# Optimization experiments

Measured on AMD Instinct MI355X. Metric: run time of the kernel, lower is better.

## Reference

```python
import jax, jax.numpy as jnp
import numpy as np

EPS = 1e-7      # geometric epsilon used in LOAI_features
BN_EPS = 1e-5   # torch BatchNorm default eps (eval mode)
B, N, C = 8, 8192, 2
S, K = 1024, 32
C_PREV = 64


def _index_points(points, idx):
    # points [B,N,C], idx [B,S,K] int -> [B,S,K,C] (torch index_points)
    return jax.vmap(lambda p, i: p[i])(points, idx)


def _conv_bn_relu(x, w, b, g, beta, m, v):
    # 1x1 Conv2d + eval-mode BatchNorm2d + ReLU. x [B,Cin,K,S], w [Cout,Cin]
    y = jnp.einsum('bcks,oc->boks', x, w) + b[None, :, None, None]
    scale = g * jax.lax.rsqrt(v + BN_EPS)
    y = (y - m[None, :, None, None]) * scale[None, :, None, None] + beta[None, :, None, None]
    return jax.nn.relu(y)


def setup_inputs() -> dict:
    key = jax.random.key(0)
    ks = jax.random.split(key, 8)
    contour = jax.random.normal(ks[0], (B, N, C), jnp.float32)
    loa = jax.random.normal(ks[1], (B, N, C), jnp.float32)
    loa = loa / (jnp.linalg.norm(loa, axis=-1, keepdims=True) + 1e-8)  # unit LOA vectors
    prev = jax.random.normal(ks[2], (B, C_PREV, N), jnp.float32)

    def lin(k, o, i):
        return jax.random.normal(k, (o, i), jnp.float32) * (1.0 / np.sqrt(i))

    d = {
        'contour_all_points': contour,
        'LOA_all_points': loa,
        'feature_maps_from_prev_layer': prev,
        # feature-enhancement MLP: 8 -> 32 -> 64
        'ew1': lin(ks[3], 32, 8), 'eb1': jnp.zeros(32), 'eg1': jnp.ones(32),
        'ebeta1': jnp.zeros(32), 'em1': jnp.zeros(32), 'ev1': jnp.ones(32),
        'ew2': lin(ks[4], 64, 32), 'eb2': jnp.zeros(64), 'eg2': jnp.ones(64),
        'ebeta2': jnp.zeros(64), 'em2': jnp.zeros(64), 'ev2': jnp.ones(64),
        # filter MLP: (64 + C_PREV)=128 -> 128 -> 256
        'fw1': lin(ks[5], 128, 64 + C_PREV), 'fb1': jnp.zeros(128), 'fg1': jnp.ones(128),
        'fbeta1': jnp.zeros(128), 'fm1': jnp.zeros(128), 'fv1': jnp.ones(128),
        'fw2': lin(ks[6], 256, 128), 'fb2': jnp.zeros(256), 'fg2': jnp.ones(256),
        'fbeta2': jnp.zeros(256), 'fm2': jnp.zeros(256), 'fv2': jnp.ones(256),
    }
    return d


def reference(contour_all_points, LOA_all_points, feature_maps_from_prev_layer,
              ew1, eb1, eg1, ebeta1, em1, ev1,
              ew2, eb2, eg2, ebeta2, em2, ev2,
              fw1, fb1, fg1, fbeta1, fm1, fv1,
              fw2, fb2, fg2, fbeta2, fm2, fv2):
    # --- downsampling: linspace indices over contour (static) ---
    new_idx = np.linspace(0, N - 1, S).astype(np.int64)              # [S]
    gidx_np = (new_idx[None, :, None] - K // 2 + np.arange(K)[None, None, :]) % N  # [1,S,K]
    gidx = jnp.broadcast_to(jnp.asarray(gidx_np), (B, S, K))

    sampled = contour_all_points[:, new_idx, :]                      # [B,S,C]
    loa_ci = LOA_all_points[:, new_idx, :][:, :, None, :]            # [B,S,1,C]

    # --- gather neighbor windows ---
    xi = _index_points(contour_all_points, gidx)                     # [B,S,K,C]
    loa_xi = _index_points(LOA_all_points, gidx)                     # [B,S,K,C]

    def sdot(a, b):
        return jnp.sum(a * b, axis=-1, keepdims=True)

    def oriented_angle(cos_a, cos_b, dotp):
        ang = jnp.arccos(jnp.clip(dotp, -1.0 + EPS, 1.0 - EPS))
        sign = jnp.where(cos_a < cos_b, 1.0, -1.0)  # equal case -> -1, as in torch
        return sign * ang

    # --- rotation-invariant features ---
    vec = xi - sampled[:, :, None, :]
    f4 = jnp.linalg.norm(vec, axis=-1, keepdims=True)                # dist ci->xi
    u = vec / (f4 + EPS)
    a1 = sdot(loa_ci, u)
    a2 = sdot(loa_xi, -u)
    f3o = oriented_angle(a1, a2, sdot(loa_xi, loa_ci))

    vecp = xi - jnp.roll(xi, 1, axis=2)
    vecp = vecp.at[:, :, 0, :].set(0.0)
    f8 = jnp.linalg.norm(vecp, axis=-1, keepdims=True)
    up = vecp / (f8 + EPS)
    loa_xim1 = jnp.roll(loa_xi, 1, axis=2).at[:, :, 0, :].set(0.0)
    a4 = sdot(up, loa_xi)
    a5 = sdot(up, loa_xim1)
    f7o = oriented_angle(a4, a5, sdot(loa_xi, loa_xim1))

    ru = jnp.roll(u, 1, axis=2).at[:, :, 0, :].set(0.0)
    d2 = jnp.arccos(jnp.clip(sdot(u, ru), -1.0 + EPS, 1.0 - EPS))

    rif = jnp.concatenate([f4, d2, a1, a2, f3o, a4, a5, f7o], axis=-1)  # [B,S,K,8]

    # --- feature enhancement MLP on [B,8,K,S] ---
    x = jnp.transpose(rif, (0, 3, 2, 1))
    x = _conv_bn_relu(x, ew1, eb1, eg1, ebeta1, em1, ev1)
    x = _conv_bn_relu(x, ew2, eb2, eg2, ebeta2, em2, ev2)            # [B,64,K,S]

    # --- group previous-layer features and concat ---
    prev_bnc = jnp.transpose(feature_maps_from_prev_layer, (0, 2, 1))  # [B,N,Cp]
    grouped_prev = _index_points(prev_bnc, gidx)                     # [B,S,K,Cp]
    grouped_prev = jnp.transpose(grouped_prev, (0, 3, 2, 1))         # [B,Cp,K,S]
    x = jnp.concatenate([x, grouped_prev], axis=1)                   # [B,128,K,S]

    # --- filter MLP + max-pool over neighbors ---
    x = _conv_bn_relu(x, fw1, fb1, fg1, fbeta1, fm1, fv1)
    x = _conv_bn_relu(x, fw2, fb2, fg2, fbeta2, fm2, fv2)            # [B,256,K,S]
    out = jnp.max(x, axis=2)                                         # [B,256,S]
    return out
```

## Files before the change

kernel.cpp:

```cpp
#include <hip/hip_runtime.h>
#include <math.h>

namespace {

constexpr int Nn = 8192;
constexpr int Ss = 1024;
constexpr float F_EPS = 1e-7f;
constexpr float F_BN_EPS = 1e-5f;

typedef __attribute__((ext_vector_type(8))) short s16x8;
typedef __attribute__((ext_vector_type(4))) float f32x4;

constexpr int WB3 = 0;
constexpr int WB4 = 32768;
constexpr int BB3 = 98304;
constexpr int BB4 = 98816;
constexpr int EW1 = 99840;
constexpr int EB1 = 100864;
constexpr int EW2 = 100992;
constexpr int EB2 = 109184;
constexpr size_t WS_NEED = 109440;

constexpr size_t CATO = 131072;
constexpr size_t PVT  = CATO + 33554432ull;
constexpr size_t WS_BIG = PVT + 8388608ull;

__device__ inline unsigned short f2bf(float f) {
  unsigned int u = __builtin_bit_cast(unsigned int, f);
  u += 0x7fffu + ((u >> 16) & 1u);
  return (unsigned short)(u >> 16);
}

__device__ inline s16x8 pack_scaled(const float* __restrict__ p, float sc) {
  const float4 w0 = *(const float4*)p;
  const float4 w1 = *(const float4*)(p + 4);
  s16x8 r;
  r[0] = (short)f2bf(w0.x * sc); r[1] = (short)f2bf(w0.y * sc);
  r[2] = (short)f2bf(w0.z * sc); r[3] = (short)f2bf(w0.w * sc);
  r[4] = (short)f2bf(w1.x * sc); r[5] = (short)f2bf(w1.y * sc);
  r[6] = (short)f2bf(w1.z * sc); r[7] = (short)f2bf(w1.w * sc);
  return r;
}

__device__ inline s16x8 prev_frag(const float* __restrict__ prev, int b, int cbase, int n) {
  const float* p = prev + (size_t)(b * 64 + cbase) * Nn + n;
  s16x8 r;
#pragma unroll
  for (int j = 0; j < 8; ++j) r[j] = (short)f2bf(p[j * Nn]);
  return r;
}

__device__ inline int ci_of(int s) {
  return (s == Ss - 1) ? (Nn - 1) : (int)(long long)((double)s * (8191.0 / 1023.0));
}

__global__ __launch_bounds__(256) void rcri_prep(
    const float* __restrict__ ew1, const float* __restrict__ eb1,
    const float* __restrict__ eg1, const float* __restrict__ ebeta1,
    const float* __restrict__ em1, const float* __restrict__ ev1,
    const float* __restrict__ ew2, const float* __restrict__ eb2,
    const float* __restrict__ eg2, const float* __restrict__ ebeta2,
    const float* __restrict__ em2, const float* __restrict__ ev2,
    const float* __restrict__ fw1, const float* __restrict__ fb1,
    const float* __restrict__ fg1, const float* __restrict__ fbeta1,
    const float* __restrict__ fm1, const float* __restrict__ fv1,
    const float* __restrict__ fw2, const float* __restrict__ fb2,
    const float* __restrict__ fg2, const float* __restrict__ fbeta2,
    const float* __restrict__ fm2, const float* __restrict__ fv2,
    unsigned char* __restrict__ ws)
{
  const int i = blockIdx.x * 256 + threadIdx.x;
  if (i < 16384) {
    const int o = i >> 7;
    const float sc = fg1[o] * rsqrtf(fv1[o] + F_BN_EPS);
    ((unsigned short*)(ws + WB3))[i] = f2bf(fw1[i] * sc);
    return;
  }
  int j = i - 16384;
  if (j < 32768) {
    const int o = j >> 7;
    const float sc = fg2[o] * rsqrtf(fv2[o] + F_BN_EPS);
    ((unsigned short*)(ws + WB4))[j] = f2bf(fw2[j] * sc);
    return;
  }
  j -= 32768;
  if (j < 128) {
    const float sc = fg1[j] * rsqrtf(fv1[j] + F_BN_EPS);
    ((float*)(ws + BB3))[j] = (fb1[j] - fm1[j]) * sc + fbeta1[j];
    return;
  }
  j -= 128;
  if (j < 256) {
    const float sc = fg2[j] * rsqrtf(fv2[j] + F_BN_EPS);
    ((float*)(ws + BB4))[j] = (fb2[j] - fm2[j]) * sc + fbeta2[j];
    return;
  }
  j -= 256;
  if (j < 256) {
    const int o = j >> 3;
    const float sc = eg1[o] * rsqrtf(ev1[o] + F_BN_EPS);
    ((float*)(ws + EW1))[j] = ew1[j] * sc;
    return;
  }
  j -= 256;
  if (j < 32) {
    const float sc = eg1[j] * rsqrtf(ev1[j] + F_BN_EPS);
    ((float*)(ws + EB1))[j] = (eb1[j] - em1[j]) * sc + ebeta1[j];
    return;
  }
  j -= 32;
  if (j < 2048) {
    const int o = j >> 5;
    const float sc = eg2[o] * rsqrtf(ev2[o] + F_BN_EPS);
    ((float*)(ws + EW2))[j] = ew2[j] * sc;
    return;
  }
  j -= 2048;
  if (j < 64) {
    const float sc = eg2[j] * rsqrtf(ev2[j] + F_BN_EPS);
    ((float*)(ws + EB2))[j] = (eb2[j] - em2[j]) * sc + ebeta2[j];
  }
}

__global__ __launch_bounds__(256) void rcri_tpose(
    const float* __restrict__ prev, unsigned char* __restrict__ ws)
{
  __shared__ unsigned short tile[128 * 72];
  const int t = threadIdx.x;
  const int b = blockIdx.x >> 6;
  const int n0 = (blockIdx.x & 63) * 128;
  const int nloc = t & 127;
  const int chalf = t >> 7;

#pragma unroll
  for (int it = 0; it < 32; ++it) {
    const int c = it * 2 + chalf;
    const float v = prev[(size_t)(b * 64 + c) * Nn + n0 + nloc];
    tile[nloc * 72 + c] = f2bf(v);
  }
  __syncthreads();

#pragma unroll
  for (int it = 0; it < 4; ++it) {
    const int idx = it * 256 + t;
    const int rn = idx >> 3;
    const int cc = idx & 7;
    const uint4 v = *(const uint4*)((const unsigned char*)tile + rn * 144 + cc * 16);
    *(uint4*)(ws + PVT + (size_t)(b * Nn + n0 + rn) * 128 + cc * 16) = v;
  }
}

__global__ __launch_bounds__(256) void rcri_k1f2(
    const float* __restrict__ contour, const float* __restrict__ loa,
    unsigned char* __restrict__ ws)
{
  __shared__ float wlds[2400];
  __shared__ __align__(16) unsigned char cstage[128 * 144];

  const int t = threadIdx.x;
  for (int j = t; j < 2400; j += 256) wlds[j] = ((const float*)(ws + EW1))[j];

  const int r = t & 127;
  const int hf = t >> 7;
  const int row = blockIdx.x * 128 + r;
  const int b = row >> 15;
  const int s = (row >> 5) & 1023;
  const int kk = row & 31;
  const int ci = ci_of(s);
  const int n = (ci - 16 + kk) & (Nn - 1);

  const float2* c2 = (const float2*)contour;
  const float2* l2 = (const float2*)loa;

  const float2 xi = c2[b * Nn + n];
  const float2 lx = l2[b * Nn + n];
  const float2 sp = c2[b * Nn + ci];
  const float2 lc = l2[b * Nn + ci];

  float2 xim1 = make_float2(0.f, 0.f), lxm1 = make_float2(0.f, 0.f);
  if (kk > 0) {
    const int np = (ci - 16 + kk - 1) & (Nn - 1);
    xim1 = c2[b * Nn + np];
    lxm1 = l2[b * Nn + np];
  }

  const float vx = xi.x - sp.x, vy = xi.y - sp.y;
  const float f4 = sqrtf(vx * vx + vy * vy);
  const float inv = 1.0f / (f4 + F_EPS);
  const float ux = vx * inv, uy = vy * inv;
  const float a1 = lc.x * ux + lc.y * uy;
  const float a2 = -(lx.x * ux + lx.y * uy);
  float dotp = lx.x * lc.x + lx.y * lc.y;
  float cl = fminf(fmaxf(dotp, -1.0f + F_EPS), 1.0f - F_EPS);
  const float f3o = (a1 < a2 ? 1.0f : -1.0f) * acosf(cl);

  float pux = 0.f, puy = 0.f;
  if (kk > 0) {
    const float pvx = xim1.x - sp.x, pvy = xim1.y - sp.y;
    const float pf4 = sqrtf(pvx * pvx + pvy * pvy);
    const float pinv = 1.0f / (pf4 + F_EPS);
    pux = pvx * pinv; puy = pvy * pinv;
  }
  const float vpx = (kk > 0) ? (xi.x - xim1.x) : 0.0f;
  const float vpy = (kk > 0) ? (xi.y - xim1.y) : 0.0f;
  const float f8 = sqrtf(vpx * vpx + vpy * vpy);
  const float invp = 1.0f / (f8 + F_EPS);
  const float upx = vpx * invp, upy = vpy * invp;
  const float a4 = upx * lx.x + upy * lx.y;
  const float a5 = upx * lxm1.x + upy * lxm1.y;
  float dotp2 = lx.x * lxm1.x + lx.y * lxm1.y;
  float cl2 = fminf(fmaxf(dotp2, -1.0f + F_EPS), 1.0f - F_EPS);
  const float f7o = (a4 < a5 ? 1.0f : -1.0f) * acosf(cl2);
  float du = ux * pux + uy * puy;
  float cl3 = fminf(fmaxf(du, -1.0f + F_EPS), 1.0f - F_EPS);
  const float d2 = acosf(cl3);

  __syncthreads();

  float h1v[32];
#pragma unroll
  for (int o = 0; o < 32; ++o) {
    const float4 w0 = *(const float4*)(wlds + o * 8);
    const float4 w1 = *(const float4*)(wlds + o * 8 + 4);
    float acc = wlds[256 + o]
      + w0.x * f4  + w0.y * d2  + w0.z * a1  + w0.w * a2
      + w1.x * f3o + w1.y * a4  + w1.z * a5  + w1.w * f7o;
    h1v[o] = fmaxf(acc, 0.f);
  }

#pragma unroll
  for (int grp = 0; grp < 4; ++grp) {
    unsigned int uu[4];
#pragma unroll
    for (int q = 0; q < 4; ++q) {
      float y2[2];
#pragma unroll
      for (int jj = 0; jj < 2; ++jj) {
        const int o = hf * 32 + grp * 8 + q * 2 + jj;
        float acc = wlds[2336 + o];
#pragma unroll
        for (int c4 = 0; c4 < 8; ++c4) {
          const float4 ww = *(const float4*)(wlds + 288 + o * 32 + c4 * 4);
          acc += ww.x * h1v[c4 * 4 + 0] + ww.y * h1v[c4 * 4 + 1]
               + ww.z * h1v[c4 * 4 + 2] + ww.w * h1v[c4 * 4 + 3];
        }
        y2[jj] = fmaxf(acc, 0.f);
      }
      uu[q] = (unsigned)f2bf(y2[0]) | ((unsigned)f2bf(y2[1]) << 16);
    }
    *(uint4*)(cstage + r * 144 + hf * 64 + grp * 16) = make_uint4(uu[0], uu[1], uu[2], uu[3]);
  }
  __syncthreads();

#pragma unroll
  for (int it = 0; it < 4; ++it) {
    const int idx = it * 256 + t;
    const int rr = idx >> 3;
    const int cc = idx & 7;
    const uint4 v = *(const uint4*)(cstage + rr * 144 + cc * 16);
    *(uint4*)(ws + CATO + (size_t)(blockIdx.x * 128 + rr) * 128 + cc * 16) = v;
  }
}

__global__ __launch_bounds__(256) void rcri_k23(
    const unsigned char* __restrict__ ws, float* __restrict__ out)
{
  __shared__ __align__(16) unsigned char h3s[32768];
  __shared__ float obuf[256 * 5];

  const int t = threadIdx.x;
  const int lane = t & 63;
  const int w = t >> 6;
  const int rl = lane & 15;
  const int g = lane >> 4;
  const int rows0 = blockIdx.x * 128;
  const int b = blockIdx.x >> 8;
  const int sbase = (blockIdx.x & 255) * 4;

  {
    const unsigned short* wb3 = (const unsigned short*)(ws + WB3);
    const float* b3p = (const float*)(ws + BB3);
    s16x8 B3[2][4];
    float bb3[2];
#pragma unroll
    for (int i = 0; i < 2; ++i) {
      const int o = (2 * w + i) * 16 + rl;
#pragma unroll
      for (int kt = 0; kt < 4; ++kt)
        B3[i][kt] = *(const s16x8*)(wb3 + o * 128 + kt * 32 + 8 * g);
      bb3[i] = b3p[o];
    }
    for (int mt = 0; mt < 8; ++mt) {
      const int row = rows0 + mt * 16 + rl;
      const int s = (row >> 5) & 1023;
      const int kk = row & 31;
      const int ci = ci_of(s);
      const int n = (ci - 16 + kk) & (Nn - 1);

      const s16x8 a0 = __builtin_bit_cast(s16x8,
          *(const uint4*)(ws + CATO + (size_t)row * 128 + 16 * g));
      const s16x8 a1 = __builtin_bit_cast(s16x8,
          *(const uint4*)(ws + CATO + (size_t)row * 128 + 64 + 16 * g));
      const s16x8 a2 = __builtin_bit_cast(s16x8,
          *(const uint4*)(ws + PVT + (size_t)(b * Nn + n) * 128 + 16 * g));
      const s16x8 a3 = __builtin_bit_cast(s16x8,
          *(const uint4*)(ws + PVT + (size_t)(b * Nn + n) * 128 + 64 + 16 * g));

#pragma unroll
      for (int i = 0; i < 2; ++i) {
        f32x4 acc = {0.f, 0.f, 0.f, 0.f};
        acc = __builtin_amdgcn_mfma_f32_16x16x32_bf16(a0, B3[i][0], acc, 0, 0, 0);
        acc = __builtin_amdgcn_mfma_f32_16x16x32_bf16(a1, B3[i][1], acc, 0, 0, 0);
        acc = __builtin_amdgcn_mfma_f32_16x16x32_bf16(a2, B3[i][2], acc, 0, 0, 0);
        acc = __builtin_amdgcn_mfma_f32_16x16x32_bf16(a3, B3[i][3], acc, 0, 0, 0);
        const int o = (2 * w + i) * 16 + rl;
#pragma unroll
        for (int r = 0; r < 4; ++r) {
          const int row2 = mt * 16 + 4 * g + r;
          const float y = fmaxf(acc[r] + bb3[i], 0.f);
          *(unsigned short*)(h3s + row2 * 256 + ((2 * o) ^ ((row2 & 15) << 4))) = f2bf(y);
        }
      }
    }
  }
  __syncthreads();

  {
    const unsigned short* wb4 = (const unsigned short*)(ws + WB4);
    const float* b4p = (const float*)(ws + BB4);
    s16x8 B4[4][4];
    float bb4[4];
#pragma unroll
    for (int ni = 0; ni < 4; ++ni) {
      const int o = (4 * w + ni) * 16 + rl;
#pragma unroll
      for (int kt = 0; kt < 4; ++kt)
        B4[ni][kt] = *(const s16x8*)(wb4 + o * 128 + kt * 32 + 8 * g);
      bb4[ni] = b4p[o];
    }
    float vmax[4] = {-INFINITY, -INFINITY, -INFINITY, -INFINITY};
    for (int mt = 0; mt < 8; ++mt) {
      const int rowl = mt * 16 + rl;
      s16x8 a[4];
#pragma unroll
      for (int kt = 0; kt < 4; ++kt)
        a[kt] = __builtin_bit_cast(s16x8,
            *(const uint4*)(h3s + rowl * 256 + ((kt * 64 + 16 * g) ^ ((rowl & 15) << 4))));
#pragma unroll
      for (int ni = 0; ni < 4; ++ni) {
        f32x4 acc = {0.f, 0.f, 0.f, 0.f};
        acc = __builtin_amdgcn_mfma_f32_16x16x32_bf16(a[0], B4[ni][0], acc, 0, 0, 0);
        acc = __builtin_amdgcn_mfma_f32_16x16x32_bf16(a[1], B4[ni][1], acc, 0, 0, 0);
        acc = __builtin_amdgcn_mfma_f32_16x16x32_bf16(a[2], B4[ni][2], acc, 0, 0, 0);
        acc = __builtin_amdgcn_mfma_f32_16x16x32_bf16(a[3], B4[ni][3], acc, 0, 0, 0);
#pragma unroll
        for (int r = 0; r < 4; ++r)
          vmax[ni] = fmaxf(vmax[ni], fmaxf(acc[r] + bb4[ni], 0.f));
      }
      if (mt & 1) {
        const int sl = mt >> 1;
#pragma unroll
        for (int ni = 0; ni < 4; ++ni) {
          float v = vmax[ni];
          v = fmaxf(v, __shfl_xor(v, 16));
          v = fmaxf(v, __shfl_xor(v, 32));
          if (g == 0) {
            const int o = (4 * w + ni) * 16 + rl;
            obuf[o * 5 + sl] = v;
          }
          vmax[ni] = -INFINITY;
        }
      }
    }
  }
  __syncthreads();
  {
    float v[4];
#pragma unroll
    for (int j = 0; j < 4; ++j) v[j] = obuf[t * 5 + j];
    float* po = out + ((size_t)(b * 256 + t) << 10) + sbase;
    float4 v0; v0.x = v[0]; v0.y = v[1]; v0.z = v[2]; v0.w = v[3];
    *(float4*)po = v0;
  }
}

template <bool P>
__global__ __launch_bounds__(256, 2) void rcri_main(
    const float* __restrict__ contour, const float* __restrict__ loa,
    const float* __restrict__ prev, const unsigned char* __restrict__ ws,
    const float* __restrict__ ew1, const float* __restrict__ eb1,
    const float* __restrict__ eg1, const float* __restrict__ ebeta1,
    const float* __restrict__ em1, const float* __restrict__ ev1,
    const float* __restrict__ ew2, const float* __restrict__ eb2,
    const float* __restrict__ eg2, const float* __restrict__ ebeta2,
    const float* __restrict__ em2, const float* __restrict__ ev2,
    const float* __restrict__ fw1, const float* __restrict__ fb1,
    const float* __restrict__ fg1, const float* __restrict__ fbeta1,
    const float* __restrict__ fm1, const float* __restrict__ fv1,
    const float* __restrict__ fw2, const float* __restrict__ fb2,
    const float* __restrict__ fg2, const float* __restrict__ fbeta2,
    const float* __restrict__ fm2, const float* __restrict__ fv2,
    float* __restrict__ out)
{
  __shared__ __align__(16) unsigned char smem[65536 + 9216];
  float* obuf = (float*)(smem + 65536);

  const int t = threadIdx.x;
  const int lane = t & 63;
  const int w = t >> 6;
  const int rl = lane & 15;
  const int g = lane >> 4;
  const int blk = blockIdx.x;
  const int b = blk >> 7;
  const int s_base = (blk & 127) << 3;

  const unsigned short* wb3 = (const unsigned short*)(ws + WB3);
  const unsigned short* wb4 = (const unsigned short*)(ws + WB4);
  const float* b3p = (const float*)(ws + BB3);
  const float* b4p = (const float*)(ws + BB4);
  const float* w1p = (const float*)(ws + EW1);
  const float* b1p = (const float*)(ws + EB1);
  const float* w2p = (const float*)(ws + EW2);
  const float* b2p = (const float*)(ws + EB2);

  const float2* c2 = (const float2*)contour;
  const float2* l2 = (const float2*)loa;

  auto cat_off = [](int m, int byte) { return m * 256 + (byte ^ ((m & 15) << 4)); };
  auto h3_off  = [](int m, int byte) { return 32768 + m * 256 + (byte ^ ((m & 15) << 4)); };

  for (int hh = 0; hh < 2; ++hh) {
    {
      const int m = t & 127;
      const int hf = t >> 7;
      const int sl4 = m >> 5, kk = m & 31;
      const int s = s_base + hh * 4 + sl4;
      const int ci = ci_of(s);
      const int n = (ci - 16 + kk) & (Nn - 1);

#pragma unroll
      for (int u = 0; u < 8; ++u) {
        const int c0 = hf * 32 + u * 4;
        const float* pp = prev + (size_t)(b * 64 + c0) * Nn + n;
        const float p0 = pp[0], p1 = pp[Nn], p2 = pp[2 * Nn], p3 = pp[3 * Nn];
        const unsigned int u0 = (unsigned)f2bf(p0) | ((unsigned)f2bf(p1) << 16);
        const unsigned int u1 = (unsigned)f2bf(p2) | ((unsigned)f2bf(p3) << 16);
        *(uint2*)(smem + cat_off(m, 128 + 2 * c0)) = make_uint2(u0, u1);
      }

      const float2 xi = c2[b * Nn + n];
      const float2 lx = l2[b * Nn + n];
      const float2 sp = c2[b * Nn + ci];
      const float2 lc = l2[b * Nn + ci];

      float2 xim1 = make_float2(0.f, 0.f), lxm1 = make_float2(0.f, 0.f);
      if (kk > 0) {
        const int np = (ci - 16 + kk - 1) & (Nn - 1);
        xim1 = c2[b * Nn + np];
        lxm1 = l2[b * Nn + np];
      }

      const float vx = xi.x - sp.x, vy = xi.y - sp.y;
      const float f4 = sqrtf(vx * vx + vy * vy);
      const float inv = 1.0f / (f4 + F_EPS);
      const float ux = vx * inv, uy = vy * inv;
      const float a1 = lc.x * ux + lc.y * uy;
      const float a2 = -(lx.x * ux + lx.y * uy);
      float dotp = lx.x * lc.x + lx.y * lc.y;
      float cl = fminf(fmaxf(dotp, -1.0f + F_EPS), 1.0f - F_EPS);
      const float f3o = (a1 < a2 ? 1.0f : -1.0f) * acosf(cl);

      float pux = 0.f, puy = 0.f;
      if (kk > 0) {
        const float pvx = xim1.x - sp.x, pvy = xim1.y - sp.y;
        const float pf4 = sqrtf(pvx * pvx + pvy * pvy);
        const float pinv = 1.0f / (pf4 + F_EPS);
        pux = pvx * pinv; puy = pvy * pinv;
      }
      const float vpx = (kk > 0) ? (xi.x - xim1.x) : 0.0f;
      const float vpy = (kk > 0) ? (xi.y - xim1.y) : 0.0f;
      const float f8 = sqrtf(vpx * vpx + vpy * vpy);
      const float invp = 1.0f / (f8 + F_EPS);
      const float upx = vpx * invp, upy = vpy * invp;
      const float a4 = upx * lx.x + upy * lx.y;
      const float a5 = upx * lxm1.x + upy * lxm1.y;
      float dotp2 = lx.x * lxm1.x + lx.y * lxm1.y;
      float cl2 = fminf(fmaxf(dotp2, -1.0f + F_EPS), 1.0f - F_EPS);
      const float f7o = (a4 < a5 ? 1.0f : -1.0f) * acosf(cl2);
      float du = ux * pux + uy * puy;
      float cl3 = fminf(fmaxf(du, -1.0f + F_EPS), 1.0f - F_EPS);
      const float d2 = acosf(cl3);

      const float rif[8] = {f4, d2, a1, a2, f3o, a4, a5, f7o};

      float h1v[32];
#pragma unroll
      for (int o = 0; o < 32; ++o) {
        float acc;
        if (P) {
          acc = b1p[o];
#pragma unroll
          for (int c = 0; c < 8; ++c) acc += w1p[o * 8 + c] * rif[c];
        } else {
          float a0 = 0.f;
#pragma unroll
          for (int c = 0; c < 8; ++c) a0 += ew1[o * 8 + c] * rif[c];
          const float sc = eg1[o] * rsqrtf(ev1[o] + F_BN_EPS);
          acc = (a0 + eb1[o] - em1[o]) * sc + ebeta1[o];
        }
        h1v[o] = fmaxf(acc, 0.f);
      }

#pragma unroll
      for (int i = 0; i < 8; ++i) {
        float yv[4];
#pragma unroll
        for (int j = 0; j < 4; ++j) {
          const int o = hf * 32 + i * 4 + j;
          float acc;
          if (P) {
            acc = b2p[o];
#pragma unroll
            for (int c = 0; c < 32; ++c) acc += w2p[o * 32 + c] * h1v[c];
          } else {
            float a0 = 0.f;
#pragma unroll
            for (int c = 0; c < 32; ++c) a0 += ew2[o * 32 + c] * h1v[c];
            const float sc = eg2[o] * rsqrtf(ev2[o] + F_BN_EPS);
            acc = (a0 + eb2[o] - em2[o]) * sc + ebeta2[o];
          }
          yv[j] = fmaxf(acc, 0.f);
        }
        const unsigned int u0 = (unsigned)f2bf(yv[0]) | ((unsigned)f2bf(yv[1]) << 16);
        const unsigned int u1 = (unsigned)f2bf(yv[2]) | ((unsigned)f2bf(yv[3]) << 16);
        *(uint2*)(smem + cat_off(m, 64 * hf + 8 * i)) = make_uint2(u0, u1);
      }
    }
    __syncthreads();

    {
      s16x8 B3[2][4];
      float bb3[2];
#pragma unroll
      for (int i = 0; i < 2; ++i) {
        const int o = (2 * w + i) * 16 + rl;
        if (P) {
#pragma unroll
          for (int kt = 0; kt < 4; ++kt)
            B3[i][kt] = *(const s16x8*)(wb3 + o * 128 + kt * 32 + 8 * g);
          bb3[i] = b3p[o];
        } else {
          const float sc = fg1[o] * rsqrtf(fv1[o] + F_BN_EPS);
#pragma unroll
          for (int kt = 0; kt < 4; ++kt)
            B3[i][kt] = pack_scaled(fw1 + o * 128 + kt * 32 + 8 * g, sc);
          bb3[i] = (fb1[o] - fm1[o]) * sc + fbeta1[o];
        }
      }
      for (int mt = 0; mt < 8; ++mt) {
        const int row = mt * 16 + rl;
        s16x8 a[4];
#pragma unroll
        for (int kt = 0; kt < 4; ++kt)
          a[kt] = __builtin_bit_cast(s16x8, *(const uint4*)(smem + cat_off(row, kt * 64 + 16 * g)));
#pragma unroll
        for (int i = 0; i < 2; ++i) {
          f32x4 acc = {0.f, 0.f, 0.f, 0.f};
          acc = __builtin_amdgcn_mfma_f32_16x16x32_bf16(a[0], B3[i][0], acc, 0, 0, 0);
          acc = __builtin_amdgcn_mfma_f32_16x16x32_bf16(a[1], B3[i][1], acc, 0, 0, 0);
          acc = __builtin_amdgcn_mfma_f32_16x16x32_bf16(a[2], B3[i][2], acc, 0, 0, 0);
          acc = __builtin_amdgcn_mfma_f32_16x16x32_bf16(a[3], B3[i][3], acc, 0, 0, 0);
          const int o = (2 * w + i) * 16 + rl;
#pragma unroll
          for (int r = 0; r < 4; ++r) {
            const float y = fmaxf(acc[r] + bb3[i], 0.f);
            *(unsigned short*)(smem + h3_off(mt * 16 + 4 * g + r, 2 * o)) = f2bf(y);
          }
        }
      }
    }
    __syncthreads();

#pragma unroll
    for (int nip = 0; nip < 2; ++nip) {
      s16x8 B4[2][4];
      float bb4[2];
#pragma unroll
      for (int q = 0; q < 2; ++q) {
        const int o = (4 * w + nip * 2 + q) * 16 + rl;
        if (P) {
#pragma unroll
          for (int kt = 0; kt < 4; ++kt)
            B4[q][kt] = *(const s16x8*)(wb4 + o * 128 + kt * 32 + 8 * g);
          bb4[q] = b4p[o];
        } else {
          const float sc = fg2[o] * rsqrtf(fv2[o] + F_BN_EPS);
#pragma unroll
          for (int kt = 0; kt < 4; ++kt)
            B4[q][kt] = pack_scaled(fw2 + o * 128 + kt * 32 + 8 * g, sc);
          bb4[q] = (fb2[o] - fm2[o]) * sc + fbeta2[o];
        }
      }
      float vm[2] = {-INFINITY, -INFINITY};
      for (int mt = 0; mt < 8; ++mt) {
        const int row = mt * 16 + rl;
        s16x8 a[4];
#pragma unroll
        for (int kt = 0; kt < 4; ++kt)
          a[kt] = __builtin_bit_cast(s16x8, *(const uint4*)(smem + h3_off(row, kt * 64 + 16 * g)));
#pragma unroll
        for (int q = 0; q < 2; ++q) {
          f32x4 acc = {0.f, 0.f, 0.f, 0.f};
          acc = __builtin_amdgcn_mfma_f32_16x16x32_bf16(a[0], B4[q][0], acc, 0, 0, 0);
          acc = __builtin_amdgcn_mfma_f32_16x16x32_bf16(a[1], B4[q][1], acc, 0, 0, 0);
          acc = __builtin_amdgcn_mfma_f32_16x16x32_bf16(a[2], B4[q][2], acc, 0, 0, 0);
          acc = __builtin_amdgcn_mfma_f32_16x16x32_bf16(a[3], B4[q][3], acc, 0, 0, 0);
#pragma unroll
          for (int r = 0; r < 4; ++r)
            vm[q] = fmaxf(vm[q], fmaxf(acc[r] + bb4[q], 0.f));
        }
        if (mt & 1) {
          const int sl = hh * 4 + (mt >> 1);
#pragma unroll
          for (int q = 0; q < 2; ++q) {
            float v = vm[q];
            v = fmaxf(v, __shfl_xor(v, 16));
            v = fmaxf(v, __shfl_xor(v, 32));
            if (g == 0) {
              const int o = (4 * w + nip * 2 + q) * 16 + rl;
              obuf[o * 9 + sl] = v;
            }
            vm[q] = -INFINITY;
          }
        }
      }
    }
  }

  __syncthreads();
  {
    float v[8];
#pragma unroll
    for (int j = 0; j < 8; ++j) v[j] = obuf[t * 9 + j];
    float* po = out + ((size_t)(b * 256 + t) << 10) + s_base;
    float4 v0; v0.x = v[0]; v0.y = v[1]; v0.z = v[2]; v0.w = v[3];
    float4 v1; v1.x = v[4]; v1.y = v[5]; v1.z = v[6]; v1.w = v[7];
    *(float4*)po = v0;
    *(float4*)(po + 4) = v1;
  }
}

}

extern "C" void kernel_launch(void* const* d_in, const int* in_sizes, int n_in,
                              void* d_out, int out_size, void* d_ws, size_t ws_size,
                              hipStream_t stream) {
  (void)in_sizes; (void)n_in; (void)out_size;

  const float* contour = (const float*)d_in[0];
  const float* loa     = (const float*)d_in[1];
  const float* prev    = (const float*)d_in[2];
  const float* ew1 = (const float*)d_in[3];
  const float* eb1 = (const float*)d_in[4];
  const float* eg1 = (const float*)d_in[5];
  const float* ebeta1 = (const float*)d_in[6];
  const float* em1 = (const float*)d_in[7];
  const float* ev1 = (const float*)d_in[8];
  const float* ew2 = (const float*)d_in[9];
  const float* eb2 = (const float*)d_in[10];
  const float* eg2 = (const float*)d_in[11];
  const float* ebeta2 = (const float*)d_in[12];
  const float* em2 = (const float*)d_in[13];
  const float* ev2 = (const float*)d_in[14];
  const float* fw1 = (const float*)d_in[15];
  const float* fb1 = (const float*)d_in[16];
  const float* fg1 = (const float*)d_in[17];
  const float* fbeta1 = (const float*)d_in[18];
  const float* fm1 = (const float*)d_in[19];
  const float* fv1 = (const float*)d_in[20];
  const float* fw2 = (const float*)d_in[21];
  const float* fb2 = (const float*)d_in[22];
  const float* fg2 = (const float*)d_in[23];
  const float* fbeta2 = (const float*)d_in[24];
  const float* fm2 = (const float*)d_in[25];
  const float* fv2 = (const float*)d_in[26];

  float* out = (float*)d_out;
  unsigned char* ws = (unsigned char*)d_ws;

  if (ws && ws_size >= WS_BIG) {
    rcri_prep<<<dim3(203), dim3(256), 0, stream>>>(
        ew1, eb1, eg1, ebeta1, em1, ev1, ew2, eb2, eg2, ebeta2, em2, ev2,
        fw1, fb1, fg1, fbeta1, fm1, fv1, fw2, fb2, fg2, fbeta2, fm2, fv2, ws);
    rcri_tpose<<<dim3(512), dim3(256), 0, stream>>>(prev, ws);
    rcri_k1f2<<<dim3(2048), dim3(256), 0, stream>>>(contour, loa, ws);
    rcri_k23<<<dim3(2048), dim3(256), 0, stream>>>(ws, out);
  } else if (ws && ws_size >= WS_NEED) {
    rcri_prep<<<dim3(203), dim3(256), 0, stream>>>(
        ew1, eb1, eg1, ebeta1, em1, ev1, ew2, eb2, eg2, ebeta2, em2, ev2,
        fw1, fb1, fg1, fbeta1, fm1, fv1, fw2, fb2, fg2, fbeta2, fm2, fv2, ws);
    rcri_main<true><<<dim3(1024), dim3(256), 0, stream>>>(
        contour, loa, prev, ws,
        ew1, eb1, eg1, ebeta1, em1, ev1, ew2, eb2, eg2, ebeta2, em2, ev2,
        fw1, fb1, fg1, fbeta1, fm1, fv1, fw2, fb2, fg2, fbeta2, fm2, fv2, out);
  } else {
    rcri_main<false><<<dim3(1024), dim3(256), 0, stream>>>(
        contour, loa, prev, ws,
        ew1, eb1, eg1, ebeta1, em1, ev1, ew2, eb2, eg2, ebeta2, em2, ev2,
        fw1, fb1, fg1, fbeta1, fm1, fv1, fw2, fb2, fg2, fbeta2, fm2, fv2, out);
  }
}
```

Measured before the change: 109.5 us.

## Permute second filter weights to pack layer-3 outputs, drop LDS weight staging

Adds a prep kernel that stores the final-layer weights with a permuted K order, so each lane can write two adjacent bf16 layer-3 outputs as one 32-bit LDS store instead of two 16-bit stores. Bias is folded into the MFMA accumulator init and the max starts at zero, which removes the per-element ReLU and bias add. The first feature kernel now reads MLP weights straight from global memory instead of staging them in LDS behind a barrier. Neighbor index math is hoisted out of the tile loop. The risks are one extra kernel launch and uncoalesced or repeated global weight reads in k1g.

```diff
diff --git a/kernel.cpp b/kernel.cpp
--- a/kernel.cpp
+++ b/kernel.cpp
@@ -23,7 +23,8 @@
 
 constexpr size_t CATO = 131072;
 constexpr size_t PVT  = CATO + 33554432ull;
-constexpr size_t WS_BIG = PVT + 8388608ull;
+constexpr size_t WB4P = PVT + 8388608ull;
+constexpr size_t WS_BIG = WB4P + 65536ull;
 
 __device__ inline unsigned short f2bf(float f) {
   unsigned int u = __builtin_bit_cast(unsigned int, f);
@@ -122,6 +123,18 @@
   }
 }
 
+__global__ __launch_bounds__(256) void rcri_prep2(
+    const float* __restrict__ fw2, const float* __restrict__ fg2,
+    const float* __restrict__ fv2, unsigned char* __restrict__ ws)
+{
+  const int j = blockIdx.x * 256 + threadIdx.x;
+  const int o = j >> 7;
+  const int jk = j & 127;
+  const int c = 32 * (jk >> 5) + 16 * (jk & 1) + ((jk & 31) >> 1);
+  const float sc = fg2[o] * rsqrtf(fv2[o] + F_BN_EPS);
+  ((unsigned short*)(ws + WB4P))[j] = f2bf(fw2[o * 128 + c] * sc);
+}
+
 __global__ __launch_bounds__(256) void rcri_tpose(
     const float* __restrict__ prev, unsigned char* __restrict__ ws)
 {
@@ -150,16 +163,18 @@
   }
 }
 
-__global__ __launch_bounds__(256) void rcri_k1f2(
+__global__ __launch_bounds__(256) void rcri_k1g(
     const float* __restrict__ contour, const float* __restrict__ loa,
     unsigned char* __restrict__ ws)
 {
-  __shared__ float wlds[2400];
   __shared__ __align__(16) unsigned char cstage[128 * 144];
 
+  const float* w1p = (const float*)(ws + EW1);
+  const float* b1p = (const float*)(ws + EB1);
+  const float* w2p = (const float*)(ws + EW2);
+  const float* b2p = (const float*)(ws + EB2);
+
   const int t = threadIdx.x;
-  for (int j = t; j < 2400; j += 256) wlds[j] = ((const float*)(ws + EW1))[j];
-
   const int r = t & 127;
   const int hf = t >> 7;
   const int row = blockIdx.x * 128 + r;
@@ -215,14 +230,12 @@
   float cl3 = fminf(fmaxf(du, -1.0f + F_EPS), 1.0f - F_EPS);
   const float d2 = acosf(cl3);
 
-  __syncthreads();
-
   float h1v[32];
 #pragma unroll
   for (int o = 0; o < 32; ++o) {
-    const float4 w0 = *(const float4*)(wlds + o * 8);
-    const float4 w1 = *(const float4*)(wlds + o * 8 + 4);
-    float acc = wlds[256 + o]
+    const float4 w0 = *(const float4*)(w1p + o * 8);
+    const float4 w1 = *(const float4*)(w1p + o * 8 + 4);
+    float acc = b1p[o]
       + w0.x * f4  + w0.y * d2  + w0.z * a1  + w0.w * a2
       + w1.x * f3o + w1.y * a4  + w1.z * a5  + w1.w * f7o;
     h1v[o] = fmaxf(acc, 0.f);
@@ -237,10 +250,10 @@
 #pragma unroll
       for (int jj = 0; jj < 2; ++jj) {
         const int o = hf * 32 + grp * 8 + q * 2 + jj;
-        float acc = wlds[2336 + o];
+        float acc = b2p[o];
 #pragma unroll
         for (int c4 = 0; c4 < 8; ++c4) {
-          const float4 ww = *(const float4*)(wlds + 288 + o * 32 + c4 * 4);
+          const float4 ww = *(const float4*)(w2p + o * 32 + c4 * 4);
           acc += ww.x * h1v[c4 * 4 + 0] + ww.y * h1v[c4 * 4 + 1]
                + ww.z * h1v[c4 * 4 + 2] + ww.w * h1v[c4 * 4 + 3];
         }
@@ -277,6 +290,13 @@
   const int b = blockIdx.x >> 8;
   const int sbase = (blockIdx.x & 255) * 4;
 
+  const unsigned char* catp = ws + CATO + (size_t)rows0 * 128;
+  const unsigned char* pvtp = ws + PVT + (size_t)b * Nn * 128;
+
+  int nbase[4];
+#pragma unroll
+  for (int q = 0; q < 4; ++q) nbase[q] = ci_of(sbase + q) - 16;
+
   {
     const unsigned short* wb3 = (const unsigned short*)(ws + WB3);
     const float* b3p = (const float*)(ws + BB3);
@@ -291,42 +311,38 @@
       bb3[i] = b3p[o];
     }
     for (int mt = 0; mt < 8; ++mt) {
-      const int row = rows0 + mt * 16 + rl;
-      const int s = (row >> 5) & 1023;
-      const int kk = row & 31;
-      const int ci = ci_of(s);
-      const int n = (ci - 16 + kk) & (Nn - 1);
-
-      const s16x8 a0 = __builtin_bit_cast(s16x8,
-          *(const uint4*)(ws + CATO + (size_t)row * 128 + 16 * g));
-      const s16x8 a1 = __builtin_bit_cast(s16x8,
-          *(const uint4*)(ws + CATO + (size_t)row * 128 + 64 + 16 * g));
-      const s16x8 a2 = __builtin_bit_cast(s16x8,
-          *(const uint4*)(ws + PVT + (size_t)(b * Nn + n) * 128 + 16 * g));
-      const s16x8 a3 = __builtin_bit_cast(s16x8,
-          *(const uint4*)(ws + PVT + (size_t)(b * Nn + n) * 128 + 64 + 16 * g));
-
-#pragma unroll
-      for (int i = 0; i < 2; ++i) {
-        f32x4 acc = {0.f, 0.f, 0.f, 0.f};
-        acc = __builtin_amdgcn_mfma_f32_16x16x32_bf16(a0, B3[i][0], acc, 0, 0, 0);
-        acc = __builtin_amdgcn_mfma_f32_16x16x32_bf16(a1, B3[i][1], acc, 0, 0, 0);
-        acc = __builtin_amdgcn_mfma_f32_16x16x32_bf16(a2, B3[i][2], acc, 0, 0, 0);
-        acc = __builtin_amdgcn_mfma_f32_16x16x32_bf16(a3, B3[i][3], acc, 0, 0, 0);
-        const int o = (2 * w + i) * 16 + rl;
-#pragma unroll
-        for (int r = 0; r < 4; ++r) {
-          const int row2 = mt * 16 + 4 * g + r;
-          const float y = fmaxf(acc[r] + bb3[i], 0.f);
-          *(unsigned short*)(h3s + row2 * 256 + ((2 * o) ^ ((row2 & 15) << 4))) = f2bf(y);
-        }
+      const int rloc = mt * 16 + rl;
+      const int n = (nbase[mt >> 1] + (mt & 1) * 16 + rl) & (Nn - 1);
+
+      const s16x8 a0 = __builtin_bit_cast(s16x8, *(const uint4*)(catp + (size_t)rloc * 128 + 16 * g));
+      const s16x8 a1 = __builtin_bit_cast(s16x8, *(const uint4*)(catp + (size_t)rloc * 128 + 64 + 16 * g));
+      const s16x8 a2 = __builtin_bit_cast(s16x8, *(const uint4*)(pvtp + (size_t)n * 128 + 16 * g));
+      const s16x8 a3 = __builtin_bit_cast(s16x8, *(const uint4*)(pvtp + (size_t)n * 128 + 64 + 16 * g));
+
+      f32x4 acc0 = {bb3[0], bb3[0], bb3[0], bb3[0]};
+      f32x4 acc1 = {bb3[1], bb3[1], bb3[1], bb3[1]};
+      acc0 = __builtin_amdgcn_mfma_f32_16x16x32_bf16(a0, B3[0][0], acc0, 0, 0, 0);
+      acc0 = __builtin_amdgcn_mfma_f32_16x16x32_bf16(a1, B3[0][1], acc0, 0, 0, 0);
+      acc0 = __builtin_amdgcn_mfma_f32_16x16x32_bf16(a2, B3[0][2], acc0, 0, 0, 0);
+      acc0 = __builtin_amdgcn_mfma_f32_16x16x32_bf16(a3, B3[0][3], acc0, 0, 0, 0);
+      acc1 = __builtin_amdgcn_mfma_f32_16x16x32_bf16(a0, B3[1][0], acc1, 0, 0, 0);
+      acc1 = __builtin_amdgcn_mfma_f32_16x16x32_bf16(a1, B3[1][1], acc1, 0, 0, 0);
+      acc1 = __builtin_amdgcn_mfma_f32_16x16x32_bf16(a2, B3[1][2], acc1, 0, 0, 0);
+      acc1 = __builtin_amdgcn_mfma_f32_16x16x32_bf16(a3, B3[1][3], acc1, 0, 0, 0);
+
+#pragma unroll
+      for (int r = 0; r < 4; ++r) {
+        const int row2 = mt * 16 + 4 * g + r;
+        const unsigned u = (unsigned)f2bf(fmaxf(acc0[r], 0.f))
+                         | ((unsigned)f2bf(fmaxf(acc1[r], 0.f)) << 16);
+        *(unsigned int*)(h3s + row2 * 256 + ((64 * w + 4 * rl) ^ ((row2 & 15) << 4))) = u;
       }
     }
   }
   __syncthreads();
 
   {
-    const unsigned short* wb4 = (const unsigned short*)(ws + WB4);
+    const unsigned short* wb4p = (const unsigned short*)(ws + WB4P);
     const float* b4p = (const float*)(ws + BB4);
     s16x8 B4[4][4];
     float bb4[4];
@@ -335,10 +351,10 @@
       const int o = (4 * w + ni) * 16 + rl;
 #pragma unroll
       for (int kt = 0; kt < 4; ++kt)
-        B4[ni][kt] = *(const s16x8*)(wb4 + o * 128 + kt * 32 + 8 * g);
+        B4[ni][kt] = *(const s16x8*)(wb4p + o * 128 + kt * 32 + 8 * g);
       bb4[ni] = b4p[o];
     }
-    float vmax[4] = {-INFINITY, -INFINITY, -INFINITY, -INFINITY};
+    float vmax[4] = {0.f, 0.f, 0.f, 0.f};
     for (int mt = 0; mt < 8; ++mt) {
       const int rowl = mt * 16 + rl;
       s16x8 a[4];
@@ -348,14 +364,14 @@
             *(const uint4*)(h3s + rowl * 256 + ((kt * 64 + 16 * g) ^ ((rowl & 15) << 4))));
 #pragma unroll
       for (int ni = 0; ni < 4; ++ni) {
-        f32x4 acc = {0.f, 0.f, 0.f, 0.f};
+        f32x4 acc = {bb4[ni], bb4[ni], bb4[ni], bb4[ni]};
         acc = __builtin_amdgcn_mfma_f32_16x16x32_bf16(a[0], B4[ni][0], acc, 0, 0, 0);
         acc = __builtin_amdgcn_mfma_f32_16x16x32_bf16(a[1], B4[ni][1], acc, 0, 0, 0);
         acc = __builtin_amdgcn_mfma_f32_16x16x32_bf16(a[2], B4[ni][2], acc, 0, 0, 0);
         acc = __builtin_amdgcn_mfma_f32_16x16x32_bf16(a[3], B4[ni][3], acc, 0, 0, 0);
 #pragma unroll
         for (int r = 0; r < 4; ++r)
-          vmax[ni] = fmaxf(vmax[ni], fmaxf(acc[r] + bb4[ni], 0.f));
+          vmax[ni] = fmaxf(vmax[ni], acc[r]);
       }
       if (mt & 1) {
         const int sl = mt >> 1;
@@ -368,7 +384,7 @@
             const int o = (4 * w + ni) * 16 + rl;
             obuf[o * 5 + sl] = v;
           }
-          vmax[ni] = -INFINITY;
+          vmax[ni] = 0.f;
         }
       }
     }
@@ -692,8 +708,9 @@
     rcri_prep<<<dim3(203), dim3(256), 0, stream>>>(
         ew1, eb1, eg1, ebeta1, em1, ev1, ew2, eb2, eg2, ebeta2, em2, ev2,
         fw1, fb1, fg1, fbeta1, fm1, fv1, fw2, fb2, fg2, fbeta2, fm2, fv2, ws);
+    rcri_prep2<<<dim3(128), dim3(256), 0, stream>>>(fw2, fg2, fv2, ws);
     rcri_tpose<<<dim3(512), dim3(256), 0, stream>>>(prev, ws);
-    rcri_k1f2<<<dim3(2048), dim3(256), 0, stream>>>(contour, loa, ws);
+    rcri_k1g<<<dim3(2048), dim3(256), 0, stream>>>(contour, loa, ws);
     rcri_k23<<<dim3(2048), dim3(256), 0, stream>>>(ws, out);
   } else if (ws && ws_size >= WS_NEED) {
     rcri_prep<<<dim3(203), dim3(256), 0, stream>>>(
```

Result: slower. 142.3 us (+30.0%).
